# Kernel optimization log

Hardware: AMD Instinct MI355X
Metric: run time of the kernel (lower is better)

Reference implementation:

```python
import jax, jax.numpy as jnp
from jax import lax
import numpy as np

B = 512

def setup_inputs() -> dict:
    key = jax.random.key(0)
    ks = jax.random.split(key, 6)
    x = jax.random.normal(ks[0], (B, 1, 28, 28), jnp.float32)
    conv1_w = jax.random.normal(ks[1], (256, 1, 9, 9), jnp.float32) * 0.05
    conv1_b = jnp.zeros((256,), jnp.float32)
    prim_w = jax.random.normal(ks[2], (32, 32, 1, 9, 9), jnp.float32) * 0.02
    prim_b = jnp.zeros((32,), jnp.float32)
    dig_W = jax.random.normal(ks[3], (1152, 8, 16), jnp.float32) * 0.1
    dig_Wb = jnp.zeros((1152, 16), jnp.float32)
    out_w = jax.random.normal(ks[4], (10, 10, 16, 1), jnp.float32) * 0.1
    out_b = jnp.zeros((10,), jnp.float32)
    return dict(x=x, conv1_w=conv1_w, conv1_b=conv1_b, prim_w=prim_w, prim_b=prim_b,
                dig_W=dig_W, dig_Wb=dig_Wb, out_w=out_w, out_b=out_b)


def _squash(s):
    # s: [B, 16, 10]; matches torch: v = ||s||_2/(1+||s||_2) * (s^T / ||s||_1)
    l2 = jnp.sqrt(jnp.sum(s * s, axis=1))[:, :, None]      # [B, 10, 1]
    l1 = jnp.sum(jnp.abs(s), axis=1)[:, :, None]            # [B, 10, 1]
    return l2 / (1.0 + l2) * (jnp.swapaxes(s, 1, 2) / l1)   # [B, 10, 16]


def reference(x, conv1_w, conv1_b, prim_w, prim_b, dig_W, dig_Wb, out_w, out_b):
    # conv1: [B,1,28,28] -> [B,256,20,20]
    out = lax.conv_general_dilated(x, conv1_w, (1, 1), 'VALID',
                                   dimension_numbers=('NCHW', 'OIHW', 'NCHW'))
    out = jax.nn.relu(out + conv1_b[None, :, None, None])
    # primary capsules: [B,32,8,20,20] -> [B,32,8,6,6]
    out1 = out.reshape(-1, 32, 8, 20, 20)
    out1 = lax.conv_general_dilated(out1, prim_w, (1, 2, 2), 'VALID',
                                    dimension_numbers=('NCDHW', 'OIDHW', 'NCDHW'))
    out1 = jax.nn.relu(out1 + prim_b[None, :, None, None, None])
    # transpose(2,-1) then reshape -> [B, 1152, 8]
    u = jnp.swapaxes(out1, 2, 4).reshape(-1, 1152, 8)
    # per-capsule affine: [B,1152,16]
    dig = jnp.einsum('bnd,nde->bne', u, dig_W) + dig_Wb
    bsz = dig.shape[0]
    # dynamic routing: b logits are never updated in the source, so
    # c = softmax(zeros, dim=1) = 1/1152 uniform, and all 3 iterations produce
    # the identical v. Computed once (same math as the original loop).
    c = jnp.full((bsz, 1152, 10), 1.0 / 1152, dtype=dig.dtype)
    s = jnp.einsum('bni,bnd->bdi', c, dig)   # [B, 16, 10]
    v = _squash(s)                            # [B, 10, 16]
    # output Conv2d(10,10,[16,1]) on v[...,None] reduces fully -> [B,10]
    logits = jnp.einsum('bik,oik->bo', v, out_w[..., 0]) + out_b
    return jax.nn.softmax(logits, axis=1)
```

## Files before the change

kernel.cpp:

```cpp
#include <hip/hip_runtime.h>
#include <math.h>


typedef __attribute__((ext_vector_type(8))) short bf16x8;
typedef __attribute__((ext_vector_type(4))) float f32x4;

__device__ inline unsigned short f2bf(float f) {
    union { float f; unsigned u; } v; v.f = f;
    unsigned r = v.u + 0x7fff + ((v.u >> 16) & 1);
    return (unsigned short)(r >> 16);
}

#define C1TN 16008

__global__ void caps_pre(const float* __restrict__ conv1_w,
                         const float* __restrict__ prim_w,
                         const float* __restrict__ dig_Wb,
                         const float* __restrict__ out_w,
                         float* __restrict__ S,
                         float* __restrict__ colsum,
                         float* __restrict__ OW,
                         unsigned short* __restrict__ c1wp2,
                         unsigned short* __restrict__ pw2,
                         int B)
{
    const int t = threadIdx.x;
    if (blockIdx.x == 468) {
        __shared__ float cs[16];
        if (t < 16) cs[t] = 0.f;
        __syncthreads();
        {
            const int k = t & 15, g = t >> 4;
            float s = 0.f;
            for (int j = 0; j < 72; ++j) s += dig_Wb[(g * 72 + j) * 16 + k];
            atomicAdd(&cs[k], s);
        }
        __syncthreads();
        if (t < 16) colsum[t] = cs[t];
        if (t >= 64 && t < 224) {
            const int idx = t - 64, o = idx >> 4, k = idx & 15;
            float s = 0.f;
            for (int i = 0; i < 10; ++i) s += out_w[(o * 10 + i) * 16 + k];
            OW[idx] = s;
        }
        return;
    }
    const int tid = blockIdx.x * 256 + t;
    if (tid < 24576) {
        const int c = tid / 96, kn = tid % 96;
        unsigned short v = 0;
        if (kn < 72) {
            const int p = kn >> 1, lo = kn & 1, ky = p >> 2, kx = 2 * (p & 3) + lo;
            v = f2bf(conv1_w[c * 81 + 9 * ky + kx]);
        } else if (kn < 81) {
            v = f2bf(conv1_w[c * 81 + 9 * (kn - 72) + 8]);
        }
        c1wp2[tid] = v;
    } else if (tid < 24576 + 87040) {
        const int j = tid - 24576;
        const int t81 = j >> 10, rem = j & 1023, o = rem >> 5, i = rem & 31;
        pw2[j] = (t81 < 81) ? f2bf(prim_w[(o * 32 + i) * 81 + t81]) : (unsigned short)0;
    } else {
        const int k = tid - 111616;
        if (k < B * 16) S[k] = 0.f;
    }
}

__global__ __launch_bounds__(256, 2) void caps_main(
    const float* __restrict__ x,
    const float* __restrict__ conv1_b,
    const float* __restrict__ prim_b,
    const float* __restrict__ dig_W,
    const unsigned short* __restrict__ c1wp2,
    const unsigned short* __restrict__ pw2,
    float* __restrict__ S)
{
    __shared__ __align__(16) unsigned short c1t[2 * C1TN];
    __shared__ __align__(16) unsigned imgp[1344];
    __shared__ unsigned short offT[64];
    __shared__ float pbs[32];

    const int b = blockIdx.x >> 2, dp = blockIdx.x & 3;
    const int d0 = dp * 2;
    const int t = threadIdx.x;
    const int wave = t >> 6, lane = t & 63, quad = lane >> 4, l16 = lane & 15;

    const float* xb = x + b * 784;
    for (int j = t; j < 1344; j += 256) {
        unsigned v = 0;
        if (j < 784) {
            const float a = xb[j];
            const int xc = j - 28 * (int)(((unsigned)j * 37450u) >> 20);
            const float c = (xc < 27) ? xb[j + 1] : 0.f;
            v = (unsigned)f2bf(a) | ((unsigned)f2bf(c) << 16);
        }
        imgp[j] = v;
    }
    if (t < 64) {
        int v;
        if (t < 32) {
            const int ky = t >> 2, kx = 2 * (t & 3);
            v = ky * 28 + kx;
        } else {
            const int k = t + 32;
            if (k < 72) {
                const int p = k >> 1, lo = k & 1, ky = p >> 2, kx = 2 * (p & 3) + lo;
                v = ky * 28 + kx;
            } else if (k < 81) {
                v = (k - 72) * 28 + 8;
            } else v = 784;
        }
        offT[t] = (unsigned short)(4 * v);
    }
    if (t < 32) pbs[t] = prim_b[t];
    __syncthreads();

    unsigned tp0[4], tp1[4], t2a[4], t2b[4];
#pragma unroll
    for (int r = 0; r < 4; ++r) {
        tp0[r] = offT[quad * 4 + r];
        tp1[r] = offT[16 + quad * 4 + r];
        t2a[r] = offT[32 + quad * 8 + 2 * r];
        t2b[r] = offT[32 + quad * 8 + 2 * r + 1];
    }

    {
        const int e = wave >> 1;
        const int d = d0 + e;
        unsigned short* dst = c1t + e * C1TN;
        const float cb0 = conv1_b[l16 * 8 + d];
        const float cb1 = conv1_b[(16 + l16) * 8 + d];
        bf16x8 Bw0[3], Bw1[3];
#pragma unroll
        for (int ks = 0; ks < 3; ++ks) {
            Bw0[ks] = *(const bf16x8*)&c1wp2[(l16 * 8 + d) * 96 + ks * 32 + quad * 8];
            Bw1[ks] = *(const bf16x8*)&c1wp2[((16 + l16) * 8 + d) * 96 + ks * 32 + quad * 8];
        }
        for (int mt = (wave & 1); mt < 25; mt += 2) {
            const int pos = mt * 16 + l16;
            const int y = (int)(((unsigned)pos * 52429u) >> 20);
            const unsigned pb4 = (unsigned)(pos + 8 * y) * 4u;
            f32x4 a0 = {0.f, 0.f, 0.f, 0.f}, a1 = {0.f, 0.f, 0.f, 0.f};
            union { unsigned u[4]; bf16x8 v; } A;
#pragma unroll
            for (int r = 0; r < 4; ++r)
                A.u[r] = *(const unsigned*)((const char*)imgp + (pb4 + tp0[r]));
            a0 = __builtin_amdgcn_mfma_f32_16x16x32_bf16(A.v, Bw0[0], a0, 0, 0, 0);
            a1 = __builtin_amdgcn_mfma_f32_16x16x32_bf16(A.v, Bw1[0], a1, 0, 0, 0);
#pragma unroll
            for (int r = 0; r < 4; ++r)
                A.u[r] = *(const unsigned*)((const char*)imgp + (pb4 + tp1[r]));
            a0 = __builtin_amdgcn_mfma_f32_16x16x32_bf16(A.v, Bw0[1], a0, 0, 0, 0);
            a1 = __builtin_amdgcn_mfma_f32_16x16x32_bf16(A.v, Bw1[1], a1, 0, 0, 0);
#pragma unroll
            for (int r = 0; r < 4; ++r) {
                const unsigned lo = *(const unsigned*)((const char*)imgp + (pb4 + t2a[r]));
                const unsigned hi = *(const unsigned*)((const char*)imgp + (pb4 + t2b[r]));
                A.u[r] = (lo & 0xFFFFu) | (hi << 16);
            }
            a0 = __builtin_amdgcn_mfma_f32_16x16x32_bf16(A.v, Bw0[2], a0, 0, 0, 0);
            a1 = __builtin_amdgcn_mfma_f32_16x16x32_bf16(A.v, Bw1[2], a1, 0, 0, 0);
#pragma unroll
            for (int r = 0; r < 4; ++r) {
                const int pr = mt * 16 + quad * 4 + r;
                const int spar = (int)((((unsigned)pr * 52429u) >> 21) & 1u);
                const int base = pr * 40 + 8 * spar;
                dst[base + l16]      = f2bf(fmaxf(a0[r] + cb0, 0.f));
                dst[base + 16 + l16] = f2bf(fmaxf(a1[r] + cb1, 0.f));
            }
        }
    }
    __syncthreads();

    const int hp = l16 >> 3, wp = l16 & 7;
    const unsigned Lbase = 80u * (unsigned)(40 * hp + 2 * wp) + 16u * quad;
    const unsigned Lh0 = Lbase + 16u * hp;
    const unsigned Lh1 = Lbase + 16u * (1 - hp);

    f32x4 pa[12];
#pragma unroll
    for (int q = 0; q < 12; ++q) pa[q] = (f32x4){0.f, 0.f, 0.f, 0.f};

    {
        const unsigned short* apbase = pw2 + l16 * 32 + quad * 8;
        int off = wave;
        bf16x8 A0 = *(const bf16x8*)(apbase + off * 1024);
        bf16x8 A1 = *(const bf16x8*)(apbase + off * 1024 + 512);
        for (; off < 81; off += 4) {
            const int noff = off + 4;
            const bf16x8 nA0 = *(const bf16x8*)(apbase + noff * 1024);
            const bf16x8 nA1 = *(const bf16x8*)(apbase + noff * 1024 + 512);
            const int ky = (off * 57) >> 9;
            const int kx = off - 9 * ky;
            const int kk = (ky >> 1) & 1;
            const unsigned soff = 80u * (unsigned)(20 * ky + kx);
            const unsigned ad = (kk ? Lh1 : Lh0) + soff;
            const char* b0 = (const char*)c1t + ad;
#pragma unroll
            for (int nt = 0; nt < 3; ++nt) {
                const bf16x8 Bf0 = *(const bf16x8*)(b0 + nt * 6400);
                const bf16x8 Bf1 = *(const bf16x8*)(b0 + nt * 6400 + 2 * C1TN);
                pa[nt]     = __builtin_amdgcn_mfma_f32_16x16x32_bf16(A0, Bf0, pa[nt],     0, 0, 0);
                pa[3 + nt] = __builtin_amdgcn_mfma_f32_16x16x32_bf16(A1, Bf0, pa[3 + nt], 0, 0, 0);
                pa[6 + nt] = __builtin_amdgcn_mfma_f32_16x16x32_bf16(A0, Bf1, pa[6 + nt], 0, 0, 0);
                pa[9 + nt] = __builtin_amdgcn_mfma_f32_16x16x32_bf16(A1, Bf1, pa[9 + nt], 0, 0, 0);
            }
            A0 = nA0; A1 = nA1;
        }
    }
    __syncthreads();

    f32x4* redbuf = (f32x4*)c1t;
    if (wave >= 2) {
#pragma unroll
        for (int q = 0; q < 12; ++q) redbuf[((wave - 2) * 12 + q) * 64 + lane] = pa[q];
    }
    __syncthreads();
    if (wave < 2) {
#pragma unroll
        for (int q = 0; q < 12; ++q) pa[q] += redbuf[(wave * 12 + q) * 64 + lane];
        if (wave == 0) {
#pragma unroll
            for (int q = 0; q < 6; ++q) redbuf[(24 + q) * 64 + lane] = pa[6 + q];
        } else {
#pragma unroll
            for (int q = 0; q < 6; ++q) redbuf[(30 + q) * 64 + lane] = pa[q];
        }
    }
    __syncthreads();

    if (wave < 2) {
        const int d = d0 + wave;
        f32x4 full[6];
#pragma unroll
        for (int q = 0; q < 6; ++q)
            full[q] = (wave == 0) ? (pa[q] + redbuf[(30 + q) * 64 + lane])
                                  : (pa[6 + q] + redbuf[(24 + q) * 64 + lane]);

        float part[16];
#pragma unroll
        for (int k = 0; k < 16; ++k) part[k] = 0.f;

        if (wp < 6) {
#pragma unroll
            for (int mt = 0; mt < 2; ++mt)
#pragma unroll
                for (int nt = 0; nt < 3; ++nt) {
                    const f32x4 u4 = full[mt * 3 + nt];
                    const int h = 2 * nt + hp;
#pragma unroll
                    for (int r = 0; r < 4; ++r) {
                        const int o = mt * 16 + quad * 4 + r;
                        const float val = fmaxf(u4[r] + pbs[o], 0.f);
                        const int nc = o * 36 + wp * 6 + h;
                        const f32x4* wd = (const f32x4*)&dig_W[(nc * 8 + d) * 16];
#pragma unroll
                        for (int m = 0; m < 4; ++m) {
                            const f32x4 wv = wd[m];
                            part[m * 4 + 0] = fmaf(val, wv[0], part[m * 4 + 0]);
                            part[m * 4 + 1] = fmaf(val, wv[1], part[m * 4 + 1]);
                            part[m * 4 + 2] = fmaf(val, wv[2], part[m * 4 + 2]);
                            part[m * 4 + 3] = fmaf(val, wv[3], part[m * 4 + 3]);
                        }
                    }
                }
        }

#pragma unroll
        for (int k = 0; k < 16; ++k) {
            float v = part[k];
            v += __shfl_xor(v, 32, 64);
            v += __shfl_xor(v, 16, 64);
            v += __shfl_xor(v, 8, 64);
            v += __shfl_xor(v, 4, 64);
            v += __shfl_xor(v, 2, 64);
            v += __shfl_xor(v, 1, 64);
            part[k] = v;
        }
        if (lane == 0) {
#pragma unroll
            for (int k = 0; k < 16; ++k) atomicAdd(&S[b * 16 + k], part[k]);
        }
    }
}

__global__ void caps_epi(const float* __restrict__ S, const float* __restrict__ colsum,
                         const float* __restrict__ OW, const float* __restrict__ out_b,
                         float* __restrict__ out, int B)
{
    const int b = blockIdx.x * 256 + threadIdx.x;
    if (b >= B) return;
    float Sv[16]; float l2 = 0.f, l1 = 0.f;
#pragma unroll
    for (int k = 0; k < 16; ++k) {
        const float s = (S[b * 16 + k] + colsum[k]) * (1.f / 1152.f);
        Sv[k] = s; l2 += s * s; l1 += fabsf(s);
    }
    l2 = sqrtf(l2);
    const float sc = l2 / (1.f + l2) / l1;
    float lg[10]; float mx = -1e30f;
#pragma unroll
    for (int o = 0; o < 10; ++o) {
        float a = out_b[o];
#pragma unroll
        for (int k = 0; k < 16; ++k) a = fmaf(Sv[k] * sc, OW[o * 16 + k], a);
        lg[o] = a; mx = fmaxf(mx, a);
    }
    float sum = 0.f;
#pragma unroll
    for (int o = 0; o < 10; ++o) { lg[o] = expf(lg[o] - mx); sum += lg[o]; }
    const float inv = 1.f / sum;
#pragma unroll
    for (int o = 0; o < 10; ++o) out[b * 10 + o] = lg[o] * inv;
}

extern "C" void kernel_launch(void* const* d_in, const int* in_sizes, int n_in,
                              void* d_out, int out_size, void* d_ws, size_t ws_size,
                              hipStream_t stream) {
    const float* x       = (const float*)d_in[0];
    const float* conv1_w = (const float*)d_in[1];
    const float* conv1_b = (const float*)d_in[2];
    const float* prim_w  = (const float*)d_in[3];
    const float* prim_b  = (const float*)d_in[4];
    const float* dig_W   = (const float*)d_in[5];
    const float* dig_Wb  = (const float*)d_in[6];
    const float* out_w   = (const float*)d_in[7];
    const float* out_b   = (const float*)d_in[8];
    float* out = (float*)d_out;

    const int B = in_sizes[0] / 784;

    char* w = (char*)d_ws;
    float* S              = (float*)(w);
    float* colsum         = (float*)(w + 32768);
    float* OW             = (float*)(w + 32832);
    unsigned short* c1wp2 = (unsigned short*)(w + 33472);
    unsigned short* pw2   = (unsigned short*)(w + 33472 + 49152);

    caps_pre<<<469, 256, 0, stream>>>(conv1_w, prim_w, dig_Wb, out_w,
                                      S, colsum, OW, c1wp2, pw2, B);
    caps_main<<<B * 4, 256, 0, stream>>>(x, conv1_b, prim_b, dig_W, c1wp2, pw2, S);
    caps_epi<<<(B + 255) / 256, 256, 0, stream>>>(S, colsum, OW, out_b, out, B);
}
```

Baseline: 182.5 us.

## Split main kernel per depth slice, halve LDS, fuse epilogue via completion counter

```diff
diff --git a/kernel.cpp b/kernel.cpp
--- a/kernel.cpp
+++ b/kernel.cpp
@@ -22,6 +22,7 @@
                          float* __restrict__ OW,
                          unsigned short* __restrict__ c1wp2,
                          unsigned short* __restrict__ pw2,
+                         unsigned int* __restrict__ cnt,
                          int B)
 {
     const int t = threadIdx.x;
@@ -59,29 +60,38 @@
     } else if (tid < 24576 + 87040) {
         const int j = tid - 24576;
         const int t81 = j >> 10, rem = j & 1023, o = rem >> 5, i = rem & 31;
-        pw2[j] = (t81 < 81) ? f2bf(prim_w[(o * 32 + i) * 81 + t81]) : (unsigned short)0;
+        const int ci = (i >> 1) + ((i & 1) << 4);
+        pw2[j] = (t81 < 81) ? f2bf(prim_w[(o * 32 + ci) * 81 + t81]) : (unsigned short)0;
     } else {
         const int k = tid - 111616;
-        if (k < B * 16) S[k] = 0.f;
+        if (k < B * 16) {
+            S[k] = 0.f;
+            if (k < B) cnt[k] = 0u;
+        }
     }
 }
 
-__global__ __launch_bounds__(256, 2) void caps_main(
+__global__ __launch_bounds__(256, 4) void caps_main(
     const float* __restrict__ x,
     const float* __restrict__ conv1_b,
     const float* __restrict__ prim_b,
     const float* __restrict__ dig_W,
     const unsigned short* __restrict__ c1wp2,
     const unsigned short* __restrict__ pw2,
-    float* __restrict__ S)
+    float* __restrict__ S,
+    const float* __restrict__ colsum,
+    const float* __restrict__ OW,
+    const float* __restrict__ out_b,
+    unsigned int* __restrict__ cnt,
+    float* __restrict__ out)
 {
-    __shared__ __align__(16) unsigned short c1t[2 * C1TN];
+    __shared__ __align__(16) unsigned short c1t[C1TN];
     __shared__ __align__(16) unsigned imgp[1344];
     __shared__ unsigned short offT[64];
     __shared__ float pbs[32];
-
-    const int b = blockIdx.x >> 2, dp = blockIdx.x & 3;
-    const int d0 = dp * 2;
+    __shared__ float sacc[64];
+
+    const int b = blockIdx.x >> 3, d = blockIdx.x & 7;
     const int t = threadIdx.x;
     const int wave = t >> 6, lane = t & 63, quad = lane >> 4, l16 = lane & 15;
 
@@ -125,9 +135,6 @@
     }
 
     {
-        const int e = wave >> 1;
-        const int d = d0 + e;
-        unsigned short* dst = c1t + e * C1TN;
         const float cb0 = conv1_b[l16 * 8 + d];
         const float cb1 = conv1_b[(16 + l16) * 8 + d];
         bf16x8 Bw0[3], Bw1[3];
@@ -136,7 +143,7 @@
             Bw0[ks] = *(const bf16x8*)&c1wp2[(l16 * 8 + d) * 96 + ks * 32 + quad * 8];
             Bw1[ks] = *(const bf16x8*)&c1wp2[((16 + l16) * 8 + d) * 96 + ks * 32 + quad * 8];
         }
-        for (int mt = (wave & 1); mt < 25; mt += 2) {
+        for (int mt = wave; mt < 25; mt += 4) {
             const int pos = mt * 16 + l16;
             const int y = (int)(((unsigned)pos * 52429u) >> 20);
             const unsigned pb4 = (unsigned)(pos + 8 * y) * 4u;
@@ -165,8 +172,9 @@
                 const int pr = mt * 16 + quad * 4 + r;
                 const int spar = (int)((((unsigned)pr * 52429u) >> 21) & 1u);
                 const int base = pr * 40 + 8 * spar;
-                dst[base + l16]      = f2bf(fmaxf(a0[r] + cb0, 0.f));
-                dst[base + 16 + l16] = f2bf(fmaxf(a1[r] + cb1, 0.f));
+                const unsigned pk = (unsigned)f2bf(fmaxf(a0[r] + cb0, 0.f))
+                                  | ((unsigned)f2bf(fmaxf(a1[r] + cb1, 0.f)) << 16);
+                *(unsigned*)&c1t[base + 2 * l16] = pk;
             }
         }
     }
@@ -177,9 +185,9 @@
     const unsigned Lh0 = Lbase + 16u * hp;
     const unsigned Lh1 = Lbase + 16u * (1 - hp);
 
-    f32x4 pa[12];
-#pragma unroll
-    for (int q = 0; q < 12; ++q) pa[q] = (f32x4){0.f, 0.f, 0.f, 0.f};
+    f32x4 pa[6];
+#pragma unroll
+    for (int q = 0; q < 6; ++q) pa[q] = (f32x4){0.f, 0.f, 0.f, 0.f};
 
     {
         const unsigned short* apbase = pw2 + l16 * 32 + quad * 8;
@@ -198,12 +206,9 @@
             const char* b0 = (const char*)c1t + ad;
 #pragma unroll
             for (int nt = 0; nt < 3; ++nt) {
-                const bf16x8 Bf0 = *(const bf16x8*)(b0 + nt * 6400);
-                const bf16x8 Bf1 = *(const bf16x8*)(b0 + nt * 6400 + 2 * C1TN);
-                pa[nt]     = __builtin_amdgcn_mfma_f32_16x16x32_bf16(A0, Bf0, pa[nt],     0, 0, 0);
-                pa[3 + nt] = __builtin_amdgcn_mfma_f32_16x16x32_bf16(A1, Bf0, pa[3 + nt], 0, 0, 0);
-                pa[6 + nt] = __builtin_amdgcn_mfma_f32_16x16x32_bf16(A0, Bf1, pa[6 + nt], 0, 0, 0);
-                pa[9 + nt] = __builtin_amdgcn_mfma_f32_16x16x32_bf16(A1, Bf1, pa[9 + nt], 0, 0, 0);
+                const bf16x8 Bf = *(const bf16x8*)(b0 + nt * 6400);
+                pa[nt]     = __builtin_amdgcn_mfma_f32_16x16x32_bf16(A0, Bf, pa[nt],     0, 0, 0);
+                pa[3 + nt] = __builtin_amdgcn_mfma_f32_16x16x32_bf16(A1, Bf, pa[3 + nt], 0, 0, 0);
             }
             A0 = nA0; A1 = nA1;
         }
@@ -211,107 +216,99 @@
     __syncthreads();
 
     f32x4* redbuf = (f32x4*)c1t;
-    if (wave >= 2) {
-#pragma unroll
-        for (int q = 0; q < 12; ++q) redbuf[((wave - 2) * 12 + q) * 64 + lane] = pa[q];
-    }
-    __syncthreads();
-    if (wave < 2) {
-#pragma unroll
-        for (int q = 0; q < 12; ++q) pa[q] += redbuf[(wave * 12 + q) * 64 + lane];
-        if (wave == 0) {
-#pragma unroll
-            for (int q = 0; q < 6; ++q) redbuf[(24 + q) * 64 + lane] = pa[6 + q];
-        } else {
-#pragma unroll
-            for (int q = 0; q < 6; ++q) redbuf[(30 + q) * 64 + lane] = pa[q];
-        }
-    }
-    __syncthreads();
-
-    if (wave < 2) {
-        const int d = d0 + wave;
-        f32x4 full[6];
-#pragma unroll
-        for (int q = 0; q < 6; ++q)
-            full[q] = (wave == 0) ? (pa[q] + redbuf[(30 + q) * 64 + lane])
-                                  : (pa[6 + q] + redbuf[(24 + q) * 64 + lane]);
-
-        float part[16];
-#pragma unroll
-        for (int k = 0; k < 16; ++k) part[k] = 0.f;
-
-        if (wp < 6) {
-#pragma unroll
-            for (int mt = 0; mt < 2; ++mt)
-#pragma unroll
-                for (int nt = 0; nt < 3; ++nt) {
-                    const f32x4 u4 = full[mt * 3 + nt];
-                    const int h = 2 * nt + hp;
-#pragma unroll
-                    for (int r = 0; r < 4; ++r) {
-                        const int o = mt * 16 + quad * 4 + r;
-                        const float val = fmaxf(u4[r] + pbs[o], 0.f);
-                        const int nc = o * 36 + wp * 6 + h;
-                        const f32x4* wd = (const f32x4*)&dig_W[(nc * 8 + d) * 16];
-#pragma unroll
-                        for (int m = 0; m < 4; ++m) {
-                            const f32x4 wv = wd[m];
-                            part[m * 4 + 0] = fmaf(val, wv[0], part[m * 4 + 0]);
-                            part[m * 4 + 1] = fmaf(val, wv[1], part[m * 4 + 1]);
-                            part[m * 4 + 2] = fmaf(val, wv[2], part[m * 4 + 2]);
-                            part[m * 4 + 3] = fmaf(val, wv[3], part[m * 4 + 3]);
-                        }
-                    }
-                }
-        }
-
-#pragma unroll
-        for (int k = 0; k < 16; ++k) {
-            float v = part[k];
-            v += __shfl_xor(v, 32, 64);
-            v += __shfl_xor(v, 16, 64);
-            v += __shfl_xor(v, 8, 64);
-            v += __shfl_xor(v, 4, 64);
-            v += __shfl_xor(v, 2, 64);
-            v += __shfl_xor(v, 1, 64);
-            part[k] = v;
-        }
-        if (lane == 0) {
-#pragma unroll
-            for (int k = 0; k < 16; ++k) atomicAdd(&S[b * 16 + k], part[k]);
-        }
-    }
-}
-
-__global__ void caps_epi(const float* __restrict__ S, const float* __restrict__ colsum,
-                         const float* __restrict__ OW, const float* __restrict__ out_b,
-                         float* __restrict__ out, int B)
-{
-    const int b = blockIdx.x * 256 + threadIdx.x;
-    if (b >= B) return;
-    float Sv[16]; float l2 = 0.f, l1 = 0.f;
+#pragma unroll
+    for (int q = 0; q < 6; ++q) redbuf[(wave * 6 + q) * 64 + lane] = pa[q];
+    __syncthreads();
+
+    float part[16];
+#pragma unroll
+    for (int k = 0; k < 16; ++k) part[k] = 0.f;
+
+#define FOLDQ(QV)                                                           \
+    {                                                                       \
+        const int q = (QV);                                                 \
+        f32x4 u4 = redbuf[q * 64 + lane];                                   \
+        u4 += redbuf[(6 + q) * 64 + lane];                                  \
+        u4 += redbuf[(12 + q) * 64 + lane];                                 \
+        u4 += redbuf[(18 + q) * 64 + lane];                                 \
+        if (wp < 6) {                                                       \
+            const int mt = (q >= 3) ? 1 : 0;                                \
+            const int nt = q - 3 * mt;                                      \
+            const int h = 2 * nt + hp;                                      \
+            _Pragma("unroll")                                               \
+            for (int r = 0; r < 4; ++r) {                                   \
+                const int o = mt * 16 + quad * 4 + r;                       \
+                const float val = fmaxf(u4[r] + pbs[o], 0.f);               \
+                const int nc = o * 36 + wp * 6 + h;                         \
+                const f32x4* wd = (const f32x4*)&dig_W[(nc * 8 + d) * 16];  \
+                _Pragma("unroll")                                           \
+                for (int m = 0; m < 4; ++m) {                               \
+                    const f32x4 wv = wd[m];                                 \
+                    part[m * 4 + 0] = fmaf(val, wv[0], part[m * 4 + 0]);    \
+                    part[m * 4 + 1] = fmaf(val, wv[1], part[m * 4 + 1]);    \
+                    part[m * 4 + 2] = fmaf(val, wv[2], part[m * 4 + 2]);    \
+                    part[m * 4 + 3] = fmaf(val, wv[3], part[m * 4 + 3]);    \
+                }                                                           \
+            }                                                               \
+        }                                                                   \
+    }
+
+    FOLDQ(wave);
+    if (wave < 2) FOLDQ(wave + 4);
+#undef FOLDQ
+
 #pragma unroll
     for (int k = 0; k < 16; ++k) {
-        const float s = (S[b * 16 + k] + colsum[k]) * (1.f / 1152.f);
-        Sv[k] = s; l2 += s * s; l1 += fabsf(s);
-    }
-    l2 = sqrtf(l2);
-    const float sc = l2 / (1.f + l2) / l1;
-    float lg[10]; float mx = -1e30f;
-#pragma unroll
-    for (int o = 0; o < 10; ++o) {
-        float a = out_b[o];
-#pragma unroll
-        for (int k = 0; k < 16; ++k) a = fmaf(Sv[k] * sc, OW[o * 16 + k], a);
-        lg[o] = a; mx = fmaxf(mx, a);
-    }
-    float sum = 0.f;
-#pragma unroll
-    for (int o = 0; o < 10; ++o) { lg[o] = expf(lg[o] - mx); sum += lg[o]; }
-    const float inv = 1.f / sum;
-#pragma unroll
-    for (int o = 0; o < 10; ++o) out[b * 10 + o] = lg[o] * inv;
+        float v = part[k];
+        v += __shfl_xor(v, 32, 64);
+        v += __shfl_xor(v, 16, 64);
+        v += __shfl_xor(v, 8, 64);
+        v += __shfl_xor(v, 4, 64);
+        v += __shfl_xor(v, 2, 64);
+        v += __shfl_xor(v, 1, 64);
+        part[k] = v;
+    }
+    if (lane == 0) {
+#pragma unroll
+        for (int k = 0; k < 16; ++k) sacc[wave * 16 + k] = part[k];
+    }
+    __syncthreads();
+    if (t < 16) {
+        const float v = sacc[t] + sacc[16 + t] + sacc[32 + t] + sacc[48 + t];
+        atomicAdd(&S[b * 16 + t], v);
+    }
+    __threadfence();
+    __syncthreads();
+
+    if (t == 0) {
+        const unsigned old = atomicAdd(&cnt[b], 1u);
+        if (old == 7u) {
+            float Sv[16]; float l2 = 0.f, l1 = 0.f;
+#pragma unroll
+            for (int k = 0; k < 16; ++k) {
+                const float sv = (__hip_atomic_load(&S[b * 16 + k], __ATOMIC_RELAXED,
+                                                    __HIP_MEMORY_SCOPE_AGENT)
+                                  + colsum[k]) * (1.f / 1152.f);
+                Sv[k] = sv; l2 += sv * sv; l1 += fabsf(sv);
+            }
+            l2 = sqrtf(l2);
+            const float sc = l2 / (1.f + l2) / l1;
+            float lg[10]; float mx = -1e30f;
+#pragma unroll
+            for (int o = 0; o < 10; ++o) {
+                float a = out_b[o];
+#pragma unroll
+                for (int k = 0; k < 16; ++k) a = fmaf(Sv[k] * sc, OW[o * 16 + k], a);
+                lg[o] = a; mx = fmaxf(mx, a);
+            }
+            float sum = 0.f;
+#pragma unroll
+            for (int o = 0; o < 10; ++o) { lg[o] = expf(lg[o] - mx); sum += lg[o]; }
+            const float inv = 1.f / sum;
+#pragma unroll
+            for (int o = 0; o < 10; ++o) out[b * 10 + o] = lg[o] * inv;
+        }
+    }
 }
 
 extern "C" void kernel_launch(void* const* d_in, const int* in_sizes, int n_in,
@@ -336,9 +333,10 @@
     float* OW             = (float*)(w + 32832);
     unsigned short* c1wp2 = (unsigned short*)(w + 33472);
     unsigned short* pw2   = (unsigned short*)(w + 33472 + 49152);
+    unsigned int* cnt     = (unsigned int*)(w + 33472 + 49152 + 174080);
 
     caps_pre<<<469, 256, 0, stream>>>(conv1_w, prim_w, dig_Wb, out_w,
-                                      S, colsum, OW, c1wp2, pw2, B);
-    caps_main<<<B * 4, 256, 0, stream>>>(x, conv1_b, prim_b, dig_W, c1wp2, pw2, S);
-    caps_epi<<<(B + 255) / 256, 256, 0, stream>>>(S, colsum, OW, out_b, out, B);
+                                      S, colsum, OW, c1wp2, pw2, cnt, B);
+    caps_main<<<B * 8, 256, 0, stream>>>(x, conv1_b, prim_b, dig_W, c1wp2, pw2,
+                                         S, colsum, OW, out_b, cnt, out);
 }
```

Result: slower. 411.5 us (+125.5%).
